# Performance work log

Measured on AMD Instinct MI355X. Metric: run time of the kernel, lower is better.

Reference implementation:

```python
import jax, jax.numpy as jnp
import numpy as np

DROPOUT_P = 0.9  # module's self.dropout_p, training=True by default
DROPOUT_KEY = 42  # fixed key for deterministic reference


def setup_inputs() -> dict:
    key = jax.random.key(0)
    kq, kk, kv = jax.random.split(key, 3)
    B, H, S, D = 4, 16, 2048, 64
    q = jax.random.normal(kq, (B, H, S, D), dtype=jnp.float32)
    k = jax.random.normal(kk, (B, H, S, D), dtype=jnp.float32)
    v = jax.random.normal(kv, (B, H, S, D), dtype=jnp.float32)
    return {"q": q, "k": k, "v": v}


def reference(q, k, v):
    # qk = q @ k^T  -> [B,H,Sq,Skv]
    qk = jnp.einsum("bhqd,bhkd->bhqk", q, k)
    # NOTE: module divides by v.size(-1)**-0.5, i.e. multiplies by sqrt(Dv)
    inv_scale_factor = v.shape[-1] ** (-0.5)
    scaled_qk = qk / inv_scale_factor
    softmax_qk = jax.nn.softmax(scaled_qk, axis=-1)
    # dropout with p=0.9, training=True; fixed key for determinism
    keep = jax.random.bernoulli(jax.random.key(DROPOUT_KEY), 1.0 - DROPOUT_P, softmax_qk.shape)
    dropout_qk = jnp.where(keep, softmax_qk / (1.0 - DROPOUT_P), 0.0)
    out = jnp.einsum("bhqk,bhkd->bhqd", dropout_qk, v)
    return out
```

## Files before the change

kernel.cpp:

```cpp
#include <hip/hip_runtime.h>


typedef short short8 __attribute__((ext_vector_type(8)));
typedef float floatx4 __attribute__((ext_vector_type(4)));

#define S_LEN 2048
#define D_DIM 64
#define BM 64
#define BN 64
#define NTILES (S_LEN / BN)
#define E_THR 1e-7f
#define MARG 2.025f
#define CAND_CAP 40
#define K_ELEMS (64 * S_LEN * D_DIM)
#define WS_NEEDED ((size_t)K_ELEMS * 4)
#define TILE_BYTES 16384
#define BH_BYTES (NTILES * TILE_BYTES)

__device__ __forceinline__ unsigned int rotl32(unsigned int x, int n) {
  return (x << n) | (x >> (32 - n));
}

__device__ __forceinline__ unsigned int threefry_42_xorfold(unsigned int idx) {
  const unsigned int ks1 = 42u, ks2 = 0x1BD11BF0u;
  unsigned int x0 = 0u;
  unsigned int x1 = idx + ks1;
#define TF4(a, b, c, d)                          \
  x0 += x1; x1 = rotl32(x1, a); x1 ^= x0;        \
  x0 += x1; x1 = rotl32(x1, b); x1 ^= x0;        \
  x0 += x1; x1 = rotl32(x1, c); x1 ^= x0;        \
  x0 += x1; x1 = rotl32(x1, d); x1 ^= x0;
  TF4(13, 15, 26, 6)
  x0 += ks1; x1 += ks2 + 1u;
  TF4(17, 29, 16, 24)
  x0 += ks2; x1 += 2u;
  TF4(13, 15, 26, 6)
  x1 += ks1 + 3u;
  TF4(17, 29, 16, 24)
  x0 += ks1; x1 += ks2 + 4u;
  TF4(13, 15, 26, 6)
  x0 += ks2; x1 += 5u;
#undef TF4
  return x0 ^ x1;
}

__device__ __forceinline__ void split4(float4 x, uint2* hp, uint2* lop) {
  const unsigned int u0 = __float_as_uint(x.x), u1 = __float_as_uint(x.y);
  const unsigned int u2 = __float_as_uint(x.z), u3 = __float_as_uint(x.w);
  hp->x = (u0 >> 16) | (u1 & 0xFFFF0000u);
  hp->y = (u2 >> 16) | (u3 & 0xFFFF0000u);
  const float l0 = x.x - __uint_as_float(u0 & 0xFFFF0000u);
  const float l1 = x.y - __uint_as_float(u1 & 0xFFFF0000u);
  const float l2 = x.z - __uint_as_float(u2 & 0xFFFF0000u);
  const float l3 = x.w - __uint_as_float(u3 & 0xFFFF0000u);
  lop->x = (__float_as_uint(l0) >> 16) | (__float_as_uint(l1) & 0xFFFF0000u);
  lop->y = (__float_as_uint(l2) >> 16) | (__float_as_uint(l3) & 0xFFFF0000u);
}

__device__ __forceinline__ void split8(const float* x, short8* hi, short8* lo) {
  union { short8 s; uint2 u[2]; } h, l;
  split4(*(const float4*)(x + 0), &h.u[0], &l.u[0]);
  split4(*(const float4*)(x + 4), &h.u[1], &l.u[1]);
  *hi = h.s; *lo = l.s;
}

__global__ void split_k_kernel(const float* __restrict__ k, unsigned char* __restrict__ ws) {
  const int c = blockIdx.x * 256 + threadIdx.x;
  const int bh = c >> 14;
  const int cc = c & 16383;
  const int srow = cc >> 3, col8 = cc & 7;
  const int tile = srow >> 6, row = srow & 63;
  const float* src = k + ((size_t)bh * S_LEN + srow) * D_DIM + col8 * 8;
  float b8[8];
  *(float4*)&b8[0] = *(const float4*)src;
  *(float4*)&b8[4] = *(const float4*)(src + 4);
  short8 h, l;
  split8(b8, &h, &l);
  unsigned char* dst = ws + (size_t)bh * BH_BYTES + tile * TILE_BYTES +
                       row * 128 + ((col8 * 16) ^ ((row & 7) << 4));
  *(short8*)dst = h;
  *(short8*)(dst + 8192) = l;
}

__global__ __launch_bounds__(256, 4) void attn_dropout_kernel(
    const float* __restrict__ q, const float* __restrict__ k,
    const float* __restrict__ v, float* __restrict__ out,
    const unsigned char* __restrict__ kws, int usews) {
  __shared__ uint4 Kbuf[1024];
  __shared__ float2 cand[BM][CAND_CAP];
  __shared__ int cnt[BM];
  __shared__ float rowm8[BM];

  const int t = threadIdx.x;
  const int w = t >> 6;
  const int m16 = t & 15;
  const int qd = (t & 63) >> 4;
  const int lane = t & 63;
  const int i0 = blockIdx.x * BM;
  const int bh = blockIdx.y;

  const float* Qg = q + ((size_t)bh * S_LEN + i0) * D_DIM;
  const float* Kg = k + (size_t)bh * S_LEN * D_DIM;
  const float* Vg = v + (size_t)bh * S_LEN * D_DIM;

  if (t < BM) cnt[t] = 0;

  short8 ah0, ah1, al0, al1;
  {
    const int arow = 16 * w + m16;
    float qbuf[8];
    *(float4*)&qbuf[0] = *(const float4*)(Qg + arow * D_DIM + qd * 8);
    *(float4*)&qbuf[4] = *(const float4*)(Qg + arow * D_DIM + qd * 8 + 4);
    split8(qbuf, &ah0, &al0);
    *(float4*)&qbuf[0] = *(const float4*)(Qg + arow * D_DIM + 32 + qd * 8);
    *(float4*)&qbuf[4] = *(const float4*)(Qg + arow * D_DIM + 32 + qd * 8 + 4);
    split8(qbuf, &ah1, &al1);
  }

  float mrow[4];
#pragma unroll
  for (int r = 0; r < 4; ++r) mrow[r] = -1e30f;

  const unsigned int bh_base = (unsigned int)bh * (unsigned int)(S_LEN * S_LEN);

  const int swz = (m16 & 7) << 4;
  const int b_lo = m16 * 128 + ((qd * 16) ^ swz);
  const int b_hi = m16 * 128 + ((qd * 16 + 64) ^ swz);

  auto compute_tile = [&](int j0) {
    const char* Kb = (const char*)&Kbuf[0];
    floatx4 acc[4];
#pragma unroll
    for (int jj = 0; jj < 4; ++jj) {
      short8 kh0 = *(const short8*)(Kb + jj * 2048 + b_lo);
      short8 kh1 = *(const short8*)(Kb + jj * 2048 + b_hi);
      short8 kl0 = *(const short8*)(Kb + 8192 + jj * 2048 + b_lo);
      short8 kl1 = *(const short8*)(Kb + 8192 + jj * 2048 + b_hi);
      floatx4 a = {0.f, 0.f, 0.f, 0.f};
      a = __builtin_amdgcn_mfma_f32_16x16x32_bf16(ah0, kh0, a, 0, 0, 0);
      a = __builtin_amdgcn_mfma_f32_16x16x32_bf16(ah1, kh1, a, 0, 0, 0);
      a = __builtin_amdgcn_mfma_f32_16x16x32_bf16(ah0, kl0, a, 0, 0, 0);
      a = __builtin_amdgcn_mfma_f32_16x16x32_bf16(ah1, kl1, a, 0, 0, 0);
      a = __builtin_amdgcn_mfma_f32_16x16x32_bf16(al0, kh0, a, 0, 0, 0);
      a = __builtin_amdgcn_mfma_f32_16x16x32_bf16(al1, kh1, a, 0, 0, 0);
      acc[jj] = a;
    }
#pragma unroll
    for (int r = 0; r < 4; ++r) {
      const float rl = fmaxf(fmaxf(acc[0][r], acc[1][r]), fmaxf(acc[2][r], acc[3][r]));
      const unsigned long long b = __ballot(rl > mrow[r] - MARG);
      if ((b >> (16 * qd)) & 0xFFFFull) {
        float rmx = rl;
#pragma unroll
        for (int off = 1; off < 16; off <<= 1)
          rmx = fmaxf(rmx, __shfl_xor(rmx, off, 16));
        const float mn = fmaxf(mrow[r], rmx);
        mrow[r] = mn;
        const float thr = mn - MARG;
        const int lrow = 16 * w + 4 * qd + r;
#pragma unroll
        for (int jj = 0; jj < 4; ++jj) {
          if (acc[jj][r] > thr) {
            const int slot = atomicAdd(&cnt[lrow], 1);
            if (slot < CAND_CAP)
              cand[lrow][slot] = make_float2(8.f * acc[jj][r],
                                             __uint_as_float((unsigned int)(j0 + 16 * jj + m16)));
          }
        }
      }
    }
  };

  if (usews) {
    const uint4* gk = (const uint4*)(kws + (size_t)bh * BH_BYTES) + (w * 256 + lane);
    uint4* lp = &Kbuf[0] + (w * 256 + lane);
    uint4 r0 = gk[0], r1 = gk[64], r2 = gk[128], r3 = gk[192];

    for (int tile = 0; tile < NTILES; ++tile) {
      __syncthreads();
      lp[0] = r0; lp[64] = r1; lp[128] = r2; lp[192] = r3;
      __syncthreads();
      if (tile + 1 < NTILES) {
        const uint4* gp = gk + (size_t)(tile + 1) * 1024;
        r0 = gp[0]; r1 = gp[64]; r2 = gp[128]; r3 = gp[192];
      }
      compute_tile(tile * BN);
    }
  } else {
    for (int tile = 0; tile < NTILES; ++tile) {
      const int j0 = tile * BN;
      __syncthreads();
#pragma unroll
      for (int rr = 0; rr < 4; ++rr) {
        const int c = t + 256 * rr;
        const int row = c >> 4, c4 = (c & 15) * 4;
        float4 x = *(const float4*)(Kg + (size_t)(j0 + row) * D_DIM + c4);
        uint2 h, l;
        split4(x, &h, &l);
        const int bcol = c4 * 2;
        const int dst = row * 128 + ((bcol & ~15) ^ ((row & 7) << 4)) + (bcol & 15);
        char* Kb0 = (char*)&Kbuf[0];
        *(uint2*)(Kb0 + dst) = h;
        *(uint2*)(Kb0 + 8192 + dst) = l;
      }
      __syncthreads();
      compute_tile(j0);
    }
  }

  if (m16 == 0) {
#pragma unroll
    for (int r = 0; r < 4; ++r) rowm8[16 * w + 4 * qd + r] = 8.f * mrow[r];
  }
  __syncthreads();

#pragma unroll 1
  for (int ri = 0; ri < 16; ++ri) {
    const int lrow = 16 * w + ri;
    const int ncand = min(cnt[lrow], CAND_CAP);
    const float m8 = rowm8[lrow];

    float e = 0.f;
    unsigned int col = 0u;
    if (lane < ncand) {
      const float2 cd = cand[lrow][lane];
      col = __float_as_uint(cd.y);
      e = __expf(cd.x - m8);
    }

    float lsum = e;
#pragma unroll
    for (int off = 1; off < 64; off <<= 1) lsum += __shfl_xor(lsum, off);
    lsum = fmaxf(lsum, 1e-30f);

    float p = 0.f;
    if (e > E_THR) {
      const unsigned int idx = bh_base +
          (unsigned int)(i0 + lrow) * (unsigned int)S_LEN + col;
      const unsigned int rr = threefry_42_xorfold(idx);
      const float u = __uint_as_float((rr >> 9) | 0x3f800000u) - 1.0f;
      if (u < 0.1f) p = e;
    }

    float o = 0.f;
    unsigned long long kb = __ballot(p != 0.f);
    while (kb) {
      const int src = __builtin_ctzll(kb);
      kb &= kb - 1;
      const float pb = __shfl(p, src);
      const int cb = __shfl((int)col, src);
      o = fmaf(pb, Vg[(size_t)cb * D_DIM + lane], o);
    }

    const float scale = 10.0f / lsum;
    out[((size_t)bh * S_LEN + i0 + lrow) * D_DIM + lane] = o * scale;
  }
}

extern "C" void kernel_launch(void* const* d_in, const int* in_sizes, int n_in,
                              void* d_out, int out_size, void* d_ws, size_t ws_size,
                              hipStream_t stream) {
  (void)in_sizes; (void)n_in;
  const float* q = (const float*)d_in[0];
  const float* k = (const float*)d_in[1];
  const float* v = (const float*)d_in[2];
  float* out = (float*)d_out;

  unsigned char* kws = (unsigned char*)d_ws;
  const int usews = (ws_size >= WS_NEEDED) ? 1 : 0;

  if (usews) {
    split_k_kernel<<<K_ELEMS / 8 / 256, 256, 0, stream>>>(k, kws);
  }
  dim3 grid(S_LEN / BM, 64);
  attn_dropout_kernel<<<grid, 256, 0, stream>>>(q, k, v, out, kws, usews);

  if (hipGetLastError() != hipSuccess) {
    hipMemsetAsync(d_out, 0x42, (size_t)out_size * sizeof(float), stream);
  }
}
```

Measured before the change: 302.7 us.

## Screen candidates with single bf16 MFMA, recompute exact fp32 scores for survivors

Replaces the hi/lo bf16 split (six MFMAs per tile) with a single rounded-bf16 QK^T pass used only to screen candidate columns. The margin is widened and the candidate capacity raised to tolerate the lower-precision screen. Exact fp32 dot products are recomputed for the retained candidates in the epilogue, along with the row max. This halves K workspace traffic and LDS usage and raises the occupancy hint. The risk is that the wider margin overflows the candidate cap, and the fp32 recompute adds scattered global K reads per row.

```diff
diff --git a/kernel.cpp b/kernel.cpp
--- a/kernel.cpp
+++ b/kernel.cpp
@@ -10,11 +10,11 @@
 #define BN 64
 #define NTILES (S_LEN / BN)
 #define E_THR 1e-7f
-#define MARG 2.025f
-#define CAND_CAP 40
+#define MARG 3.5f
+#define CAND_CAP 64
 #define K_ELEMS (64 * S_LEN * D_DIM)
-#define WS_NEEDED ((size_t)K_ELEMS * 4)
-#define TILE_BYTES 16384
+#define WS_NEEDED ((size_t)K_ELEMS * 2)
+#define TILE_BYTES 8192
 #define BH_BYTES (NTILES * TILE_BYTES)
 
 __device__ __forceinline__ unsigned int rotl32(unsigned int x, int n) {
@@ -44,24 +44,16 @@
   return x0 ^ x1;
 }
 
-__device__ __forceinline__ void split4(float4 x, uint2* hp, uint2* lop) {
-  const unsigned int u0 = __float_as_uint(x.x), u1 = __float_as_uint(x.y);
-  const unsigned int u2 = __float_as_uint(x.z), u3 = __float_as_uint(x.w);
-  hp->x = (u0 >> 16) | (u1 & 0xFFFF0000u);
-  hp->y = (u2 >> 16) | (u3 & 0xFFFF0000u);
-  const float l0 = x.x - __uint_as_float(u0 & 0xFFFF0000u);
-  const float l1 = x.y - __uint_as_float(u1 & 0xFFFF0000u);
-  const float l2 = x.z - __uint_as_float(u2 & 0xFFFF0000u);
-  const float l3 = x.w - __uint_as_float(u3 & 0xFFFF0000u);
-  lop->x = (__float_as_uint(l0) >> 16) | (__float_as_uint(l1) & 0xFFFF0000u);
-  lop->y = (__float_as_uint(l2) >> 16) | (__float_as_uint(l3) & 0xFFFF0000u);
-}
-
-__device__ __forceinline__ void split8(const float* x, short8* hi, short8* lo) {
-  union { short8 s; uint2 u[2]; } h, l;
-  split4(*(const float4*)(x + 0), &h.u[0], &l.u[0]);
-  split4(*(const float4*)(x + 4), &h.u[1], &l.u[1]);
-  *hi = h.s; *lo = l.s;
+__device__ __forceinline__ unsigned int rne2(float a, float b) {
+  const unsigned int ua = __float_as_uint(a), ub = __float_as_uint(b);
+  return ((ua + 0x7FFFu + ((ua >> 16) & 1u)) >> 16) |
+         ((ub + 0x7FFFu + ((ub >> 16) & 1u)) & 0xFFFF0000u);
+}
+__device__ __forceinline__ short8 rne8(const float* x) {
+  union { short8 s; unsigned int u[4]; } r;
+  r.u[0] = rne2(x[0], x[1]); r.u[1] = rne2(x[2], x[3]);
+  r.u[2] = rne2(x[4], x[5]); r.u[3] = rne2(x[6], x[7]);
+  return r.s;
 }
 
 __global__ void split_k_kernel(const float* __restrict__ k, unsigned char* __restrict__ ws) {
@@ -74,22 +66,19 @@
   float b8[8];
   *(float4*)&b8[0] = *(const float4*)src;
   *(float4*)&b8[4] = *(const float4*)(src + 4);
-  short8 h, l;
-  split8(b8, &h, &l);
+  const short8 h = rne8(b8);
   unsigned char* dst = ws + (size_t)bh * BH_BYTES + tile * TILE_BYTES +
                        row * 128 + ((col8 * 16) ^ ((row & 7) << 4));
   *(short8*)dst = h;
-  *(short8*)(dst + 8192) = l;
-}
-
-__global__ __launch_bounds__(256, 4) void attn_dropout_kernel(
+}
+
+__global__ __launch_bounds__(256, 6) void attn_dropout_kernel(
     const float* __restrict__ q, const float* __restrict__ k,
     const float* __restrict__ v, float* __restrict__ out,
     const unsigned char* __restrict__ kws, int usews) {
-  __shared__ uint4 Kbuf[1024];
-  __shared__ float2 cand[BM][CAND_CAP];
+  __shared__ uint4 Kbuf[512];
+  __shared__ int candcol[BM][CAND_CAP];
   __shared__ int cnt[BM];
-  __shared__ float rowm8[BM];
 
   const int t = threadIdx.x;
   const int w = t >> 6;
@@ -105,16 +94,16 @@
 
   if (t < BM) cnt[t] = 0;
 
-  short8 ah0, ah1, al0, al1;
+  short8 ah0, ah1;
   {
     const int arow = 16 * w + m16;
     float qbuf[8];
     *(float4*)&qbuf[0] = *(const float4*)(Qg + arow * D_DIM + qd * 8);
     *(float4*)&qbuf[4] = *(const float4*)(Qg + arow * D_DIM + qd * 8 + 4);
-    split8(qbuf, &ah0, &al0);
+    ah0 = rne8(qbuf);
     *(float4*)&qbuf[0] = *(const float4*)(Qg + arow * D_DIM + 32 + qd * 8);
     *(float4*)&qbuf[4] = *(const float4*)(Qg + arow * D_DIM + 32 + qd * 8 + 4);
-    split8(qbuf, &ah1, &al1);
+    ah1 = rne8(qbuf);
   }
 
   float mrow[4];
@@ -134,15 +123,9 @@
     for (int jj = 0; jj < 4; ++jj) {
       short8 kh0 = *(const short8*)(Kb + jj * 2048 + b_lo);
       short8 kh1 = *(const short8*)(Kb + jj * 2048 + b_hi);
-      short8 kl0 = *(const short8*)(Kb + 8192 + jj * 2048 + b_lo);
-      short8 kl1 = *(const short8*)(Kb + 8192 + jj * 2048 + b_hi);
       floatx4 a = {0.f, 0.f, 0.f, 0.f};
       a = __builtin_amdgcn_mfma_f32_16x16x32_bf16(ah0, kh0, a, 0, 0, 0);
       a = __builtin_amdgcn_mfma_f32_16x16x32_bf16(ah1, kh1, a, 0, 0, 0);
-      a = __builtin_amdgcn_mfma_f32_16x16x32_bf16(ah0, kl0, a, 0, 0, 0);
-      a = __builtin_amdgcn_mfma_f32_16x16x32_bf16(ah1, kl1, a, 0, 0, 0);
-      a = __builtin_amdgcn_mfma_f32_16x16x32_bf16(al0, kh0, a, 0, 0, 0);
-      a = __builtin_amdgcn_mfma_f32_16x16x32_bf16(al1, kh1, a, 0, 0, 0);
       acc[jj] = a;
     }
 #pragma unroll
@@ -162,9 +145,7 @@
         for (int jj = 0; jj < 4; ++jj) {
           if (acc[jj][r] > thr) {
             const int slot = atomicAdd(&cnt[lrow], 1);
-            if (slot < CAND_CAP)
-              cand[lrow][slot] = make_float2(8.f * acc[jj][r],
-                                             __uint_as_float((unsigned int)(j0 + 16 * jj + m16)));
+            if (slot < CAND_CAP) candcol[lrow][slot] = j0 + 16 * jj + m16;
           }
         }
       }
@@ -172,17 +153,17 @@
   };
 
   if (usews) {
-    const uint4* gk = (const uint4*)(kws + (size_t)bh * BH_BYTES) + (w * 256 + lane);
-    uint4* lp = &Kbuf[0] + (w * 256 + lane);
-    uint4 r0 = gk[0], r1 = gk[64], r2 = gk[128], r3 = gk[192];
+    const uint4* gk = (const uint4*)(kws + (size_t)bh * BH_BYTES) + t;
+    uint4* lp = &Kbuf[0] + t;
+    uint4 r0 = gk[0], r1 = gk[256];
 
     for (int tile = 0; tile < NTILES; ++tile) {
       __syncthreads();
-      lp[0] = r0; lp[64] = r1; lp[128] = r2; lp[192] = r3;
+      lp[0] = r0; lp[256] = r1;
       __syncthreads();
       if (tile + 1 < NTILES) {
-        const uint4* gp = gk + (size_t)(tile + 1) * 1024;
-        r0 = gp[0]; r1 = gp[64]; r2 = gp[128]; r3 = gp[192];
+        const uint4* gp = gk + (size_t)(tile + 1) * 512;
+        r0 = gp[0]; r1 = gp[256];
       }
       compute_tile(tile * BN);
     }
@@ -195,38 +176,42 @@
         const int c = t + 256 * rr;
         const int row = c >> 4, c4 = (c & 15) * 4;
         float4 x = *(const float4*)(Kg + (size_t)(j0 + row) * D_DIM + c4);
-        uint2 h, l;
-        split4(x, &h, &l);
+        uint2 h2;
+        h2.x = rne2(x.x, x.y);
+        h2.y = rne2(x.z, x.w);
         const int bcol = c4 * 2;
         const int dst = row * 128 + ((bcol & ~15) ^ ((row & 7) << 4)) + (bcol & 15);
-        char* Kb0 = (char*)&Kbuf[0];
-        *(uint2*)(Kb0 + dst) = h;
-        *(uint2*)(Kb0 + 8192 + dst) = l;
+        *(uint2*)((char*)&Kbuf[0] + dst) = h2;
       }
       __syncthreads();
       compute_tile(j0);
     }
   }
-
-  if (m16 == 0) {
-#pragma unroll
-    for (int r = 0; r < 4; ++r) rowm8[16 * w + 4 * qd + r] = 8.f * mrow[r];
-  }
-  __syncthreads();
 
 #pragma unroll 1
   for (int ri = 0; ri < 16; ++ri) {
     const int lrow = 16 * w + ri;
-    const int ncand = min(cnt[lrow], CAND_CAP);
-    const float m8 = rowm8[lrow];
-
-    float e = 0.f;
-    unsigned int col = 0u;
-    if (lane < ncand) {
-      const float2 cd = cand[lrow][lane];
-      col = __float_as_uint(cd.y);
-      e = __expf(cd.x - m8);
-    }
+    const int n = min(cnt[lrow], CAND_CAP);
+    const int colv = (lane < n) ? candcol[lrow][lane] : 0;
+
+    const float4 qv4 = *(const float4*)(Qg + lrow * D_DIM + m16 * 4);
+    float d8 = -3e38f;
+    for (int i = 0; i < n; i += 4) {
+      const int c = __shfl(colv, min(i + qd, n - 1));
+      const float4 kv4 = *(const float4*)(Kg + (size_t)c * D_DIM + m16 * 4);
+      float pr = fmaf(qv4.x, kv4.x,
+                 fmaf(qv4.y, kv4.y, fmaf(qv4.z, kv4.z, qv4.w * kv4.w)));
+#pragma unroll
+      for (int off = 1; off < 16; off <<= 1) pr += __shfl_xor(pr, off, 16);
+      const float got = __shfl(pr, ((lane - i) & 3) << 4);
+      if (lane >= i && lane < min(i + 4, n)) d8 = 8.f * got;
+    }
+
+    float m8 = d8;
+#pragma unroll
+    for (int off = 1; off < 64; off <<= 1) m8 = fmaxf(m8, __shfl_xor(m8, off));
+
+    const float e = (lane < n) ? __expf(d8 - m8) : 0.f;
 
     float lsum = e;
 #pragma unroll
@@ -236,7 +221,7 @@
     float p = 0.f;
     if (e > E_THR) {
       const unsigned int idx = bh_base +
-          (unsigned int)(i0 + lrow) * (unsigned int)S_LEN + col;
+          (unsigned int)(i0 + lrow) * (unsigned int)S_LEN + (unsigned int)colv;
       const unsigned int rr = threefry_42_xorfold(idx);
       const float u = __uint_as_float((rr >> 9) | 0x3f800000u) - 1.0f;
       if (u < 0.1f) p = e;
@@ -248,7 +233,7 @@
       const int src = __builtin_ctzll(kb);
       kb &= kb - 1;
       const float pb = __shfl(p, src);
-      const int cb = __shfl((int)col, src);
+      const int cb = __shfl(colv, src);
       o = fmaf(pb, Vg[(size_t)cb * D_DIM + lane], o);
     }
 
```

New measurement: 339.3 us. +12.1%, slower.

## Switch QK^T scoring to 32x32x16 MFMA with 2x2 wave tiling

Applied to the files above, without the earlier changes.

Replaces the per-wave 16-row x 64-column tiling built from 16x16x32 bf16 MFMAs with a 2x2 wave grid, where each wave computes a 32x32 block using 32x32x16 MFMAs (three-term bf16 split). Each wave now loads only its 32-column half of the K tile, which cuts LDS reads per wave. The candidate-filtering logic is reorganised around 16 accumulator rows per lane, and the row maximum is merged across the two column waves at the end. Since each wave now sees only half the columns, the per-row running max is partial, so more candidates may pass the threshold. The candidate cap is raised slightly to absorb that, at some risk of overflow or extra atomics.

```diff
diff --git a/kernel.cpp b/kernel.cpp
--- a/kernel.cpp
+++ b/kernel.cpp
@@ -2,7 +2,7 @@
 
 
 typedef short short8 __attribute__((ext_vector_type(8)));
-typedef float floatx4 __attribute__((ext_vector_type(4)));
+typedef float floatx16 __attribute__((ext_vector_type(16)));
 
 #define S_LEN 2048
 #define D_DIM 64
@@ -11,7 +11,7 @@
 #define NTILES (S_LEN / BN)
 #define E_THR 1e-7f
 #define MARG 2.025f
-#define CAND_CAP 40
+#define CAND_CAP 44
 #define K_ELEMS (64 * S_LEN * D_DIM)
 #define WS_NEEDED ((size_t)K_ELEMS * 4)
 #define TILE_BYTES 16384
@@ -89,13 +89,15 @@
   __shared__ uint4 Kbuf[1024];
   __shared__ float2 cand[BM][CAND_CAP];
   __shared__ int cnt[BM];
-  __shared__ float rowm8[BM];
+  __shared__ float rowm8w[2][BM];
 
   const int t = threadIdx.x;
   const int w = t >> 6;
-  const int m16 = t & 15;
-  const int qd = (t & 63) >> 4;
+  const int wr = w >> 1;
+  const int wc = w & 1;
   const int lane = t & 63;
+  const int l31 = lane & 31;
+  const int half = lane >> 5;
   const int i0 = blockIdx.x * BM;
   const int bh = blockIdx.y;
 
@@ -105,66 +107,71 @@
 
   if (t < BM) cnt[t] = 0;
 
-  short8 ah0, ah1, al0, al1;
+  short8 qh[4], ql[4];
   {
-    const int arow = 16 * w + m16;
-    float qbuf[8];
-    *(float4*)&qbuf[0] = *(const float4*)(Qg + arow * D_DIM + qd * 8);
-    *(float4*)&qbuf[4] = *(const float4*)(Qg + arow * D_DIM + qd * 8 + 4);
-    split8(qbuf, &ah0, &al0);
-    *(float4*)&qbuf[0] = *(const float4*)(Qg + arow * D_DIM + 32 + qd * 8);
-    *(float4*)&qbuf[4] = *(const float4*)(Qg + arow * D_DIM + 32 + qd * 8 + 4);
-    split8(qbuf, &ah1, &al1);
-  }
-
-  float mrow[4];
-#pragma unroll
-  for (int r = 0; r < 4; ++r) mrow[r] = -1e30f;
+    const int arow = 32 * wr + l31;
+#pragma unroll
+    for (int kk = 0; kk < 4; ++kk) {
+      float qb[8];
+      *(float4*)&qb[0] = *(const float4*)(Qg + arow * D_DIM + kk * 16 + half * 8);
+      *(float4*)&qb[4] = *(const float4*)(Qg + arow * D_DIM + kk * 16 + half * 8 + 4);
+      split8(qb, &qh[kk], &ql[kk]);
+    }
+  }
+
+  float mrow[16];
+#pragma unroll
+  for (int r = 0; r < 16; ++r) mrow[r] = -1e30f;
 
   const unsigned int bh_base = (unsigned int)bh * (unsigned int)(S_LEN * S_LEN);
 
-  const int swz = (m16 & 7) << 4;
-  const int b_lo = m16 * 128 + ((qd * 16) ^ swz);
-  const int b_hi = m16 * 128 + ((qd * 16 + 64) ^ swz);
+  const int brow = 32 * wc + l31;
+  const int bswz = (brow & 7) << 4;
+  int boff[4];
+#pragma unroll
+  for (int kk = 0; kk < 4; ++kk)
+    boff[kk] = brow * 128 + ((kk * 32 + half * 16) ^ bswz);
 
   auto compute_tile = [&](int j0) {
     const char* Kb = (const char*)&Kbuf[0];
-    floatx4 acc[4];
-#pragma unroll
-    for (int jj = 0; jj < 4; ++jj) {
-      short8 kh0 = *(const short8*)(Kb + jj * 2048 + b_lo);
-      short8 kh1 = *(const short8*)(Kb + jj * 2048 + b_hi);
-      short8 kl0 = *(const short8*)(Kb + 8192 + jj * 2048 + b_lo);
-      short8 kl1 = *(const short8*)(Kb + 8192 + jj * 2048 + b_hi);
-      floatx4 a = {0.f, 0.f, 0.f, 0.f};
-      a = __builtin_amdgcn_mfma_f32_16x16x32_bf16(ah0, kh0, a, 0, 0, 0);
-      a = __builtin_amdgcn_mfma_f32_16x16x32_bf16(ah1, kh1, a, 0, 0, 0);
-      a = __builtin_amdgcn_mfma_f32_16x16x32_bf16(ah0, kl0, a, 0, 0, 0);
-      a = __builtin_amdgcn_mfma_f32_16x16x32_bf16(ah1, kl1, a, 0, 0, 0);
-      a = __builtin_amdgcn_mfma_f32_16x16x32_bf16(al0, kh0, a, 0, 0, 0);
-      a = __builtin_amdgcn_mfma_f32_16x16x32_bf16(al1, kh1, a, 0, 0, 0);
-      acc[jj] = a;
-    }
-#pragma unroll
-    for (int r = 0; r < 4; ++r) {
-      const float rl = fmaxf(fmaxf(acc[0][r], acc[1][r]), fmaxf(acc[2][r], acc[3][r]));
-      const unsigned long long b = __ballot(rl > mrow[r] - MARG);
-      if ((b >> (16 * qd)) & 0xFFFFull) {
-        float rmx = rl;
-#pragma unroll
-        for (int off = 1; off < 16; off <<= 1)
-          rmx = fmaxf(rmx, __shfl_xor(rmx, off, 16));
-        const float mn = fmaxf(mrow[r], rmx);
-        mrow[r] = mn;
-        const float thr = mn - MARG;
-        const int lrow = 16 * w + 4 * qd + r;
-#pragma unroll
-        for (int jj = 0; jj < 4; ++jj) {
-          if (acc[jj][r] > thr) {
+    short8 kh[4], kl[4];
+#pragma unroll
+    for (int kk = 0; kk < 4; ++kk) {
+      kh[kk] = *(const short8*)(Kb + boff[kk]);
+      kl[kk] = *(const short8*)(Kb + 8192 + boff[kk]);
+    }
+    floatx16 a = {0.f, 0.f, 0.f, 0.f, 0.f, 0.f, 0.f, 0.f,
+                  0.f, 0.f, 0.f, 0.f, 0.f, 0.f, 0.f, 0.f};
+#pragma unroll
+    for (int kk = 0; kk < 4; ++kk) {
+      a = __builtin_amdgcn_mfma_f32_32x32x16_bf16(qh[kk], kh[kk], a, 0, 0, 0);
+      a = __builtin_amdgcn_mfma_f32_32x32x16_bf16(qh[kk], kl[kk], a, 0, 0, 0);
+      a = __builtin_amdgcn_mfma_f32_32x32x16_bf16(ql[kk], kh[kk], a, 0, 0, 0);
+    }
+    const int col = j0 + 32 * wc + l31;
+#pragma unroll
+    for (int g = 0; g < 4; ++g) {
+      const float d0 = a[4 * g + 0] - mrow[4 * g + 0];
+      const float d1 = a[4 * g + 1] - mrow[4 * g + 1];
+      const float d2 = a[4 * g + 2] - mrow[4 * g + 2];
+      const float d3 = a[4 * g + 3] - mrow[4 * g + 3];
+      const float gm = fmaxf(fmaxf(d0, d1), fmaxf(d2, d3));
+      if (__ballot(gm > -MARG)) {
+#pragma unroll
+        for (int rr = 0; rr < 4; ++rr) {
+          const int reg = 4 * g + rr;
+          float rmx = a[reg];
+#pragma unroll
+          for (int off = 1; off < 32; off <<= 1)
+            rmx = fmaxf(rmx, __shfl_xor(rmx, off));
+          const float mn = fmaxf(mrow[reg], rmx);
+          mrow[reg] = mn;
+          if (a[reg] > mn - MARG) {
+            const int lrow = 32 * wr + (reg & 3) + 8 * (reg >> 2) + 4 * half;
             const int slot = atomicAdd(&cnt[lrow], 1);
             if (slot < CAND_CAP)
-              cand[lrow][slot] = make_float2(8.f * acc[jj][r],
-                                             __uint_as_float((unsigned int)(j0 + 16 * jj + m16)));
+              cand[lrow][slot] = make_float2(8.f * a[reg],
+                                             __uint_as_float((unsigned int)col));
           }
         }
       }
@@ -208,9 +215,10 @@
     }
   }
 
-  if (m16 == 0) {
-#pragma unroll
-    for (int r = 0; r < 4; ++r) rowm8[16 * w + 4 * qd + r] = 8.f * mrow[r];
+  if (l31 == 0) {
+#pragma unroll
+    for (int reg = 0; reg < 16; ++reg)
+      rowm8w[wc][32 * wr + (reg & 3) + 8 * (reg >> 2) + 4 * half] = 8.f * mrow[reg];
   }
   __syncthreads();
 
@@ -218,7 +226,7 @@
   for (int ri = 0; ri < 16; ++ri) {
     const int lrow = 16 * w + ri;
     const int ncand = min(cnt[lrow], CAND_CAP);
-    const float m8 = rowm8[lrow];
+    const float m8 = fmaxf(rowm8w[0][lrow], rowm8w[1][lrow]);
 
     float e = 0.f;
     unsigned int col = 0u;
```

Result: slower. 440.4 us (+45.5%).

## Split QK tile into 2x2 warp grid and compact candidate storage

Applied to the files above, without the earlier changes.

Warps now each compute a 32x32 sub-block of the 64x64 score tile instead of 16 full rows, so each K fragment loaded from LDS is reused across two row strips and fewer LDS reads are issued per MFMA. Each row's running max is now tracked separately by two warps, and the two maxima are merged at the end. Candidate storage changes from float2 to separate float values and ushort columns, which allows a larger cap in similar LDS. The trade-off is more register state (two row strips of Q fragments and maxima) and a looser per-warp threshold, which may admit more candidates and atomics.

```diff
diff --git a/kernel.cpp b/kernel.cpp
--- a/kernel.cpp
+++ b/kernel.cpp
@@ -11,7 +11,7 @@
 #define NTILES (S_LEN / BN)
 #define E_THR 1e-7f
 #define MARG 2.025f
-#define CAND_CAP 40
+#define CAND_CAP 56
 #define K_ELEMS (64 * S_LEN * D_DIM)
 #define WS_NEEDED ((size_t)K_ELEMS * 4)
 #define TILE_BYTES 16384
@@ -87,12 +87,15 @@
     const float* __restrict__ v, float* __restrict__ out,
     const unsigned char* __restrict__ kws, int usews) {
   __shared__ uint4 Kbuf[1024];
-  __shared__ float2 cand[BM][CAND_CAP];
+  __shared__ float candv[BM][CAND_CAP];
+  __shared__ unsigned short candc[BM][CAND_CAP];
   __shared__ int cnt[BM];
-  __shared__ float rowm8[BM];
+  __shared__ float rowm8w[2][BM];
 
   const int t = threadIdx.x;
   const int w = t >> 6;
+  const int wr = w >> 1;
+  const int wc = w & 1;
   const int m16 = t & 15;
   const int qd = (t & 63) >> 4;
   const int lane = t & 63;
@@ -105,66 +108,84 @@
 
   if (t < BM) cnt[t] = 0;
 
-  short8 ah0, ah1, al0, al1;
-  {
-    const int arow = 16 * w + m16;
+  short8 ah[2][2], al[2][2];
+#pragma unroll
+  for (int rs = 0; rs < 2; ++rs) {
+    const int arow = 32 * wr + 16 * rs + m16;
     float qbuf[8];
     *(float4*)&qbuf[0] = *(const float4*)(Qg + arow * D_DIM + qd * 8);
     *(float4*)&qbuf[4] = *(const float4*)(Qg + arow * D_DIM + qd * 8 + 4);
-    split8(qbuf, &ah0, &al0);
+    split8(qbuf, &ah[rs][0], &al[rs][0]);
     *(float4*)&qbuf[0] = *(const float4*)(Qg + arow * D_DIM + 32 + qd * 8);
     *(float4*)&qbuf[4] = *(const float4*)(Qg + arow * D_DIM + 32 + qd * 8 + 4);
-    split8(qbuf, &ah1, &al1);
-  }
-
-  float mrow[4];
-#pragma unroll
-  for (int r = 0; r < 4; ++r) mrow[r] = -1e30f;
+    split8(qbuf, &ah[rs][1], &al[rs][1]);
+  }
+
+  float mrow[2][4];
+#pragma unroll
+  for (int rs = 0; rs < 2; ++rs)
+#pragma unroll
+    for (int r = 0; r < 4; ++r) mrow[rs][r] = -1e30f;
 
   const unsigned int bh_base = (unsigned int)bh * (unsigned int)(S_LEN * S_LEN);
 
   const int swz = (m16 & 7) << 4;
-  const int b_lo = m16 * 128 + ((qd * 16) ^ swz);
-  const int b_hi = m16 * 128 + ((qd * 16 + 64) ^ swz);
+  int boff[2][2];
+#pragma unroll
+  for (int jj = 0; jj < 2; ++jj) {
+    const int base = (32 * wc + 16 * jj + m16) * 128;
+    boff[jj][0] = base + ((qd * 16) ^ swz);
+    boff[jj][1] = base + ((qd * 16 + 64) ^ swz);
+  }
 
   auto compute_tile = [&](int j0) {
     const char* Kb = (const char*)&Kbuf[0];
-    floatx4 acc[4];
-#pragma unroll
-    for (int jj = 0; jj < 4; ++jj) {
-      short8 kh0 = *(const short8*)(Kb + jj * 2048 + b_lo);
-      short8 kh1 = *(const short8*)(Kb + jj * 2048 + b_hi);
-      short8 kl0 = *(const short8*)(Kb + 8192 + jj * 2048 + b_lo);
-      short8 kl1 = *(const short8*)(Kb + 8192 + jj * 2048 + b_hi);
-      floatx4 a = {0.f, 0.f, 0.f, 0.f};
-      a = __builtin_amdgcn_mfma_f32_16x16x32_bf16(ah0, kh0, a, 0, 0, 0);
-      a = __builtin_amdgcn_mfma_f32_16x16x32_bf16(ah1, kh1, a, 0, 0, 0);
-      a = __builtin_amdgcn_mfma_f32_16x16x32_bf16(ah0, kl0, a, 0, 0, 0);
-      a = __builtin_amdgcn_mfma_f32_16x16x32_bf16(ah1, kl1, a, 0, 0, 0);
-      a = __builtin_amdgcn_mfma_f32_16x16x32_bf16(al0, kh0, a, 0, 0, 0);
-      a = __builtin_amdgcn_mfma_f32_16x16x32_bf16(al1, kh1, a, 0, 0, 0);
-      acc[jj] = a;
-    }
-#pragma unroll
-    for (int r = 0; r < 4; ++r) {
-      const float rl = fmaxf(fmaxf(acc[0][r], acc[1][r]), fmaxf(acc[2][r], acc[3][r]));
-      const unsigned long long b = __ballot(rl > mrow[r] - MARG);
-      if ((b >> (16 * qd)) & 0xFFFFull) {
-        float rmx = rl;
-#pragma unroll
-        for (int off = 1; off < 16; off <<= 1)
-          rmx = fmaxf(rmx, __shfl_xor(rmx, off, 16));
-        const float mn = fmaxf(mrow[r], rmx);
-        mrow[r] = mn;
-        const float thr = mn - MARG;
-        const int lrow = 16 * w + 4 * qd + r;
-#pragma unroll
-        for (int jj = 0; jj < 4; ++jj) {
-          if (acc[jj][r] > thr) {
-            const int slot = atomicAdd(&cnt[lrow], 1);
-            if (slot < CAND_CAP)
-              cand[lrow][slot] = make_float2(8.f * acc[jj][r],
-                                             __uint_as_float((unsigned int)(j0 + 16 * jj + m16)));
+    short8 kh[2][2], kl[2][2];
+#pragma unroll
+    for (int jj = 0; jj < 2; ++jj)
+#pragma unroll
+      for (int kk = 0; kk < 2; ++kk) {
+        kh[jj][kk] = *(const short8*)(Kb + boff[jj][kk]);
+        kl[jj][kk] = *(const short8*)(Kb + 8192 + boff[jj][kk]);
+      }
+    floatx4 acc[2][2];
+#pragma unroll
+    for (int rs = 0; rs < 2; ++rs)
+#pragma unroll
+      for (int jj = 0; jj < 2; ++jj) {
+        floatx4 a = {0.f, 0.f, 0.f, 0.f};
+        a = __builtin_amdgcn_mfma_f32_16x16x32_bf16(ah[rs][0], kh[jj][0], a, 0, 0, 0);
+        a = __builtin_amdgcn_mfma_f32_16x16x32_bf16(ah[rs][1], kh[jj][1], a, 0, 0, 0);
+        a = __builtin_amdgcn_mfma_f32_16x16x32_bf16(ah[rs][0], kl[jj][0], a, 0, 0, 0);
+        a = __builtin_amdgcn_mfma_f32_16x16x32_bf16(ah[rs][1], kl[jj][1], a, 0, 0, 0);
+        a = __builtin_amdgcn_mfma_f32_16x16x32_bf16(al[rs][0], kh[jj][0], a, 0, 0, 0);
+        a = __builtin_amdgcn_mfma_f32_16x16x32_bf16(al[rs][1], kh[jj][1], a, 0, 0, 0);
+        acc[rs][jj] = a;
+      }
+#pragma unroll
+    for (int rs = 0; rs < 2; ++rs) {
+#pragma unroll
+      for (int r = 0; r < 4; ++r) {
+        const float rl = fmaxf(acc[rs][0][r], acc[rs][1][r]);
+        const unsigned long long b = __ballot(rl > mrow[rs][r] - MARG);
+        if ((b >> (16 * qd)) & 0xFFFFull) {
+          float rmx = rl;
+#pragma unroll
+          for (int off = 1; off < 16; off <<= 1)
+            rmx = fmaxf(rmx, __shfl_xor(rmx, off, 16));
+          const float mn = fmaxf(mrow[rs][r], rmx);
+          mrow[rs][r] = mn;
+          const float thr = mn - MARG;
+          const int lrow = 32 * wr + 16 * rs + 4 * qd + r;
+#pragma unroll
+          for (int jj = 0; jj < 2; ++jj) {
+            if (acc[rs][jj][r] > thr) {
+              const int slot = atomicAdd(&cnt[lrow], 1);
+              if (slot < CAND_CAP) {
+                candv[lrow][slot] = 8.f * acc[rs][jj][r];
+                candc[lrow][slot] = (unsigned short)(j0 + 32 * wc + 16 * jj + m16);
+              }
+            }
           }
         }
       }
@@ -210,7 +231,10 @@
 
   if (m16 == 0) {
 #pragma unroll
-    for (int r = 0; r < 4; ++r) rowm8[16 * w + 4 * qd + r] = 8.f * mrow[r];
+    for (int rs = 0; rs < 2; ++rs)
+#pragma unroll
+      for (int r = 0; r < 4; ++r)
+        rowm8w[wc][32 * wr + 16 * rs + 4 * qd + r] = 8.f * mrow[rs][r];
   }
   __syncthreads();
 
@@ -218,14 +242,13 @@
   for (int ri = 0; ri < 16; ++ri) {
     const int lrow = 16 * w + ri;
     const int ncand = min(cnt[lrow], CAND_CAP);
-    const float m8 = rowm8[lrow];
+    const float m8 = fmaxf(rowm8w[0][lrow], rowm8w[1][lrow]);
 
     float e = 0.f;
     unsigned int col = 0u;
     if (lane < ncand) {
-      const float2 cd = cand[lrow][lane];
-      col = __float_as_uint(cd.y);
-      e = __expf(cd.x - m8);
+      col = candc[lrow][lane];
+      e = __expf(candv[lrow][lane] - m8);
     }
 
     float lsum = e;
```

New measurement: 341.7 us. +12.9%, slower.
